# Kernel optimization log

Hardware: AMD Instinct MI355X
Metric: run time of the kernel (lower is better)

The kernel has to match this reference:

```python
import jax, jax.numpy as jnp
import numpy as np

B, T, C, D, P = 8, 512, 32, 128, 1024
EPS = 1e-5

def setup_inputs() -> dict:
    key = jax.random.key(0)
    ks = jax.random.split(key, 11)
    s = 1.0 / np.sqrt(D)
    inp = {
        'x': jax.random.normal(ks[0], (B, T, C, D), jnp.float32),
        'x_mask': jax.random.randint(ks[1], (B, T, C), 0, 2) == 1,
        'p_mask': jax.random.randint(ks[2], (B, T, C), 0, 2) == 1,
        'pos': jax.random.randint(ks[3], (B, T, C), 0, P),
        'pe': jax.random.normal(ks[4], (P, D // 2, 2), jnp.float32),  # complex rpe as [re, im]
        'imp': jax.random.randint(ks[5], (B, T), 0, C),
        'idx_c': jax.random.randint(ks[6], (B, T, C), 0, C),
        'wq_w': jax.random.normal(ks[7], (D, D), jnp.float32) * s,
        'wq_b': jnp.zeros((D,), jnp.float32),
        'wk_w': jax.random.normal(ks[8], (D, D), jnp.float32) * s,
        'wk_b': jnp.zeros((D,), jnp.float32),
        'wv_w': jax.random.normal(ks[9], (D, D), jnp.float32) * s,
        'wv_b': jnp.zeros((D,), jnp.float32),
        'ls_gamma': 1e-5 * jnp.ones((D,), jnp.float32),
        'ln_gamma': jnp.ones((D,), jnp.float32),
        'ln_beta': jnp.zeros((D,), jnp.float32),
    }
    return inp


def _rotate(z, r):
    # z: (b,t,c,d) real; r: (b,t,c,d/2,2) complex multiplier [re,im]
    b, t, c, d = z.shape
    zr = z.reshape(b, t, c, d // 2, 2)
    re = zr[..., 0] * r[..., 0] - zr[..., 1] * r[..., 1]
    im = zr[..., 0] * r[..., 1] + zr[..., 1] * r[..., 0]
    return jnp.stack([re, im], axis=-1).reshape(b, t, c, d)


def reference(x, x_mask, p_mask, pos, pe, imp, idx_c,
              wq_w, wq_b, wk_w, wk_b, wv_w, wv_b,
              ls_gamma, ln_gamma, ln_beta):
    b, t, c, d = x.shape
    # channel selection gather: where x_mask, use per-token important channel
    imp_rep = jnp.broadcast_to(imp[:, :, None], (b, t, c))
    idx = jnp.where(x_mask, imp_rep, idx_c)            # (b,t,c)
    xg = jnp.take_along_axis(x, idx[..., None], axis=2)  # (b,t,c,d)
    # QKV projections (torch Linear: x @ W.T + b)
    q = xg @ wq_w.T + wq_b
    k = xg @ wk_w.T + wk_b
    v = xg @ wv_w.T + wv_b
    # relative PE complex rotation on q,k
    r = pe[pos]                                        # (b,t,c,d/2,2)
    q = _rotate(q, r)
    k = _rotate(k, r)
    # (b,c,t,d) layout; channel acts as head
    qt = q.transpose(0, 2, 1, 3)
    kt = k.transpose(0, 2, 1, 3)
    vt = v.transpose(0, 2, 1, 3)
    scores = jnp.einsum('bcqd,bckd->bcqk', qt, kt) / jnp.sqrt(jnp.float32(d))
    pm = p_mask.transpose(0, 2, 1)                     # (b,c,t)
    mask = pm[:, :, :, None] | pm[:, :, None, :]       # (b,c,t,t)
    attn = jax.nn.softmax(jnp.where(mask, -jnp.inf, scores), axis=-1)
    attn = jnp.nan_to_num(attn)
    xm = x_mask.transpose(0, 2, 1)                     # (b,c,t)
    weight = jnp.where(xm, 1.0 / t, 1.0)
    out = jnp.einsum('bcmn,bcnd->bmcd', attn * weight[:, :, None, :], vt)  # (b,t,c,d)
    # norm_first=False: LN(x + layer_scale(out))
    y = x + ls_gamma * out
    mu = jnp.mean(y, axis=-1, keepdims=True)
    var = jnp.mean(jnp.square(y - mu), axis=-1, keepdims=True)
    return (y - mu) / jnp.sqrt(var + EPS) * ln_gamma + ln_beta
```

## Files before the change

### kernel.cpp

```cpp
#include <hip/hip_runtime.h>
#include <hip/hip_bf16.h>

#define Bb 8
#define Tt 512
#define Cc 32
#define Dd 128
#define SCALE 0.08838834764831845f
#define SROW 520

typedef unsigned int u32;
typedef __hip_bfloat16 bf16;
typedef __attribute__((ext_vector_type(8))) short short8;
typedef __attribute__((ext_vector_type(4))) short short4v;
typedef __attribute__((ext_vector_type(4))) float floatx4;

__device__ __forceinline__ short f2bf(float f) {
    __hip_bfloat16 h = __float2bfloat16(f);
    return *(short*)&h;
}
__device__ __forceinline__ float bf2f(short s) {
    return __uint_as_float(((u32)(unsigned short)s) << 16);
}

__global__ __launch_bounds__(256)
void k_wconv(const float* __restrict__ wq, const float* __restrict__ wk,
             const float* __restrict__ wv, short* __restrict__ Wb)
{
    int g = blockIdx.x * 256 + threadIdx.x;
    int mat = g >> 14, rem = g & 16383;
    const float* src = (mat == 0) ? wq : (mat == 1) ? wk : wv;
    Wb[g] = f2bf(src[rem]);
}

__global__ __launch_bounds__(256)
void k_qkvm(const float* __restrict__ x, const int* __restrict__ xm,
            const int* __restrict__ pos, const float* __restrict__ pe,
            const int* __restrict__ imp, const int* __restrict__ idxc,
            const short* __restrict__ Wb,
            const float* __restrict__ bq, const float* __restrict__ bk,
            const float* __restrict__ bv,
            short* __restrict__ qb, short* __restrict__ kb, short* __restrict__ vb)
{
    const int R0  = blockIdx.x * 64;
    const int b   = R0 >> 14;
    const int t0  = (R0 >> 5) & 511;
    const int tid = threadIdx.x;
    const int w    = tid >> 6;
    const int lane = tid & 63;
    const int quad = lane >> 4;
    const int m    = lane & 15;

    __shared__ short xg[64 * 136];
    __shared__ short ot[64 * 392];

#pragma unroll
    for (int i = 0; i < 8; ++i) {
        int u   = tid + i * 256;
        int row = u >> 5, seg = u & 31;
        int R   = R0 + row;
        int idx = xm[R] ? imp[R >> 5] : idxc[R];
        float4 v = *(const float4*)(x + ((long)(R >> 5) * Cc + idx) * Dd + seg * 4);
        short4v s = {f2bf(v.x), f2bf(v.y), f2bf(v.z), f2bf(v.w)};
        *(short4v*)&xg[row * 136 + seg * 4] = s;
    }

    short8 wf[6][4];
    float  bias_v[6];
#pragma unroll
    for (int mat = 0; mat < 3; ++mat) {
        const float* bp = (mat == 0) ? bq : (mat == 1) ? bk : bv;
#pragma unroll
        for (int h = 0; h < 2; ++h) {
            int sl = mat * 2 + h;
            int ct = h * 4 + w;
            bias_v[sl] = bp[ct * 16 + m];
#pragma unroll
            for (int kk = 0; kk < 4; ++kk)
                wf[sl][kk] = *(const short8*)(Wb + ((long)mat * 128 + ct * 16 + m) * 128
                                              + kk * 32 + quad * 8);
        }
    }
    __syncthreads();

    for (int rt = 0; rt < 4; ++rt) {
        short8 af[4];
#pragma unroll
        for (int kk = 0; kk < 4; ++kk)
            af[kk] = *(const short8*)&xg[(rt * 16 + m) * 136 + kk * 32 + quad * 8];

        floatx4 acc[6];
#pragma unroll
        for (int sl = 0; sl < 6; ++sl) acc[sl] = (floatx4){0.f, 0.f, 0.f, 0.f};
#pragma unroll
        for (int kk = 0; kk < 4; ++kk)
#pragma unroll
            for (int sl = 0; sl < 6; ++sl)
                acc[sl] = __builtin_amdgcn_mfma_f32_16x16x32_bf16(af[kk], wf[sl][kk], acc[sl], 0, 0, 0);

        int po[4];
#pragma unroll
        for (int r = 0; r < 4; ++r) po[r] = pos[R0 + rt * 16 + quad * 4 + r];

#pragma unroll
        for (int sl = 0; sl < 6; ++sl) {
            int mat = sl >> 1;
            int ct  = (sl & 1) * 4 + w;
            int d   = ct * 16 + m;
#pragma unroll
            for (int r = 0; r < 4; ++r) {
                float v = acc[sl][r] + bias_v[sl];
                float p = __shfl_xor(v, 1, 64);
                if (mat < 2) {
                    const float* rp = pe + ((long)po[r] * (Dd / 2) + (d >> 1)) * 2;
                    float r0 = rp[0], r1 = rp[1];
                    v = (d & 1) ? fmaf(p, r1, v * r0) : fmaf(v, r0, -(p * r1));
                    if (mat == 0) v *= SCALE;
                }
                ot[(rt * 16 + quad * 4 + r) * 392 + mat * 128 + d] = f2bf(v);
            }
        }
    }
    __syncthreads();

    short* const mats[3] = {qb, kb, vb};
#pragma unroll
    for (int mat = 0; mat < 3; ++mat) {
        short* dst = mats[mat];
#pragma unroll
        for (int i = 0; i < 4; ++i) {
            int g = tid + i * 256;
            int n = g >> 4, off = (g & 15) * 8;
            int c = n & 31, tl = n >> 5;
            *(short8*)(dst + (((long)(b * Cc + c) * Tt) + t0 + tl) * Dd + off) =
                *(const short8*)&ot[n * 392 + mat * 128 + off];
        }
    }
}

__global__ __launch_bounds__(256)
void k_vt(const short* __restrict__ vb, const int* __restrict__ xm,
          short* __restrict__ vt)
{
    const int head = blockIdx.y;
    const int b    = head >> 5;
    const int c    = head & 31;
    const int t0   = blockIdx.x * 64;
    const int tid  = threadIdx.x;

    __shared__ short tile[64 * 136];
    __shared__ float wks[64];

    if (tid < 64)
        wks[tid] = xm[((long)b * Tt + t0 + tid) * Cc + c] ? (1.0f / Tt) : 1.0f;

    const short* src = vb + ((long)head * Tt + t0) * Dd;
#pragma unroll
    for (int i = 0; i < 4; ++i) {
        int u = tid + i * 256;
        int row = u >> 4, col = (u & 15) * 8;
        *(short8*)&tile[row * 136 + col] = *(const short8*)(src + row * Dd + col);
    }
    __syncthreads();

    short* dst = vt + (long)head * Dd * Tt + t0;
#pragma unroll
    for (int i = 0; i < 4; ++i) {
        int u = tid + i * 256;
        int d = u >> 3, t8 = (u & 7) * 8;
        short8 v;
#pragma unroll
        for (int j = 0; j < 8; ++j)
            v[j] = f2bf(bf2f(tile[(t8 + j) * 136 + d]) * wks[t8 + j]);
        *(short8*)(dst + (long)d * Tt + t8) = v;
    }
}

__global__ __launch_bounds__(512, 4)
void k_attn(const short* __restrict__ qb, const short* __restrict__ kbp,
            const short* __restrict__ vtp, const float* __restrict__ x,
            const int* __restrict__ pm,
            const float* __restrict__ lsg, const float* __restrict__ lng,
            const float* __restrict__ lnb, float* __restrict__ out)
{
    const int l    = blockIdx.y * 256 + blockIdx.x;
    const int xcd  = l & 7;
    const int sws  = l >> 3;
    const int hh   = sws & 7;
    const int tl   = (sws >> 3) & 7;
    const int gg   = sws >> 6;
    const int head = xcd + ((gg * 8 + hh) << 3);
    const int b    = head >> 5;
    const int c    = head & 31;
    const int qt0  = tl * 64;
    const int tid  = threadIdx.x;
    const int w    = tid >> 6;
    const int lane = tid & 63;
    const int quad = lane >> 4;
    const int m    = lane & 15;
    const int d    = w * 16 + m;

    __shared__ short S[64 * SROW];
    __shared__ u32   pkbits[16];
    __shared__ float rlS[64];
    __shared__ float ps1[8][64];
    __shared__ float ps2[8][64];
    __shared__ float mrs[64][2];

    {
        bool v = pm[((long)b * Tt + tid) * Cc + c] != 0;
        unsigned long long bal = __ballot(v);
        if (lane == 0) {
            pkbits[w * 2]     = (u32)bal;
            pkbits[w * 2 + 1] = (u32)(bal >> 32);
        }
    }

    short8 qf[4][4];
#pragma unroll
    for (int qt = 0; qt < 4; ++qt)
#pragma unroll
        for (int kk = 0; kk < 4; ++kk)
            qf[qt][kk] = *(const short8*)(qb + ((long)head * Tt + qt0 + qt * 16 + m) * Dd
                                          + kk * 32 + quad * 8);
    __syncthreads();

    for (int ch = 0; ch < 4; ++ch) {
        int kt = ch * 128 + w * 16 + m;
        const short* kp = kbp + ((long)head * Tt + kt) * Dd + quad * 8;
        floatx4 sc[4];
#pragma unroll
        for (int qt = 0; qt < 4; ++qt) sc[qt] = (floatx4){0.f, 0.f, 0.f, 0.f};
#pragma unroll
        for (int kk = 0; kk < 4; ++kk) {
            short8 bk = *(const short8*)(kp + kk * 32);
            __builtin_amdgcn_s_setprio(1);
#pragma unroll
            for (int qt = 0; qt < 4; ++qt)
                sc[qt] = __builtin_amdgcn_mfma_f32_16x16x32_bf16(qf[qt][kk], bk, sc[qt], 0, 0, 0);
            __builtin_amdgcn_s_setprio(0);
        }
        bool masked = (pkbits[kt >> 5] >> (kt & 31)) & 1;
#pragma unroll
        for (int qt = 0; qt < 4; ++qt)
#pragma unroll
            for (int r = 0; r < 4; ++r)
                S[(qt * 16 + quad * 4 + r) * SROW + kt] = f2bf(masked ? -1e30f : sc[qt][r]);
    }

    const short* vbase = vtp + (long)head * Dd * Tt + ((long)d) * Tt + quad * 8;
    short8 bvbuf[8];
#pragma unroll
    for (int kv = 0; kv < 8; ++kv)
        bvbuf[kv] = *(const short8*)(vbase + kv * 32);

    float xv[4][4];
#pragma unroll
    for (int qt = 0; qt < 4; ++qt)
#pragma unroll
        for (int r = 0; r < 4; ++r) {
            int row = qt * 16 + quad * 4 + r;
            xv[qt][r] = x[(((long)b * Tt + qt0 + row) * Cc + c) * Dd + d];
        }
    __syncthreads();

    {
        int qi = tid >> 3, part = tid & 7;
        short* rowp = &S[qi * SROW + part * 8];
        short8 sv[8];
#pragma unroll
        for (int j = 0; j < 8; ++j) sv[j] = *(short8*)&rowp[j * 64];
        float mx = -1e30f;
#pragma unroll
        for (int j = 0; j < 8; ++j)
#pragma unroll
            for (int e = 0; e < 8; ++e) mx = fmaxf(mx, bf2f(sv[j][e]));
        mx = fmaxf(mx, __shfl_xor(mx, 1, 64));
        mx = fmaxf(mx, __shfl_xor(mx, 2, 64));
        mx = fmaxf(mx, __shfl_xor(mx, 4, 64));
        float lsum = 0.f;
#pragma unroll
        for (int j = 0; j < 8; ++j)
#pragma unroll
            for (int e = 0; e < 8; ++e) {
                float s = bf2f(sv[j][e]);
                float ex = (s <= -1e29f) ? 0.f : __expf(s - mx);
                sv[j][e] = f2bf(ex);
                lsum += ex;
            }
#pragma unroll
        for (int j = 0; j < 8; ++j) *(short8*)&rowp[j * 64] = sv[j];
        lsum += __shfl_xor(lsum, 1, 64);
        lsum += __shfl_xor(lsum, 2, 64);
        lsum += __shfl_xor(lsum, 4, 64);
        if (part == 0) {
            int t = qt0 + qi;
            bool qmask = (pkbits[t >> 5] >> (t & 31)) & 1;
            rlS[qi] = (lsum > 0.f && !qmask) ? 1.0f / lsum : 0.f;
        }
    }
    __syncthreads();

    floatx4 oa[4];
#pragma unroll
    for (int qt = 0; qt < 4; ++qt) oa[qt] = (floatx4){0.f, 0.f, 0.f, 0.f};

#pragma unroll
    for (int kv = 0; kv < 16; ++kv) {
        short8 bv = bvbuf[kv & 7];
        if (kv < 8) bvbuf[kv] = *(const short8*)(vbase + (kv + 8) * 32);
        __builtin_amdgcn_s_setprio(1);
#pragma unroll
        for (int qt = 0; qt < 4; ++qt) {
            short8 ap = *(const short8*)&S[(qt * 16 + m) * SROW + kv * 32 + quad * 8];
            oa[qt] = __builtin_amdgcn_mfma_f32_16x16x32_bf16(ap, bv, oa[qt], 0, 0, 0);
        }
        __builtin_amdgcn_s_setprio(0);
    }

    const float lg = lsg[d];
    float yv[4][4];
#pragma unroll
    for (int qt = 0; qt < 4; ++qt)
#pragma unroll
        for (int r = 0; r < 4; ++r) {
            int row = qt * 16 + quad * 4 + r;
            float val = oa[qt][r] * rlS[row];
            float y = xv[qt][r] + lg * val;
            yv[qt][r] = y;
        }
#pragma unroll
    for (int qt = 0; qt < 4; ++qt)
#pragma unroll
        for (int r = 0; r < 4; ++r) {
            float a = yv[qt][r], bb = yv[qt][r] * yv[qt][r];
            a += __shfl_xor(a, 1, 64); bb += __shfl_xor(bb, 1, 64);
            a += __shfl_xor(a, 2, 64); bb += __shfl_xor(bb, 2, 64);
            a += __shfl_xor(a, 4, 64); bb += __shfl_xor(bb, 4, 64);
            a += __shfl_xor(a, 8, 64); bb += __shfl_xor(bb, 8, 64);
            if (m == 0) {
                ps1[w][qt * 16 + quad * 4 + r] = a;
                ps2[w][qt * 16 + quad * 4 + r] = bb;
            }
        }
    __syncthreads();
    if (tid < 64) {
        float a = 0.f, bb = 0.f;
#pragma unroll
        for (int wv = 0; wv < 8; ++wv) { a += ps1[wv][tid]; bb += ps2[wv][tid]; }
        float mean = a * (1.0f / Dd);
        float var  = bb * (1.0f / Dd) - mean * mean;
        mrs[tid][0] = mean;
        mrs[tid][1] = rsqrtf(var + 1e-5f);
    }
    __syncthreads();

    const float g = lng[d], be = lnb[d];
#pragma unroll
    for (int qt = 0; qt < 4; ++qt)
#pragma unroll
        for (int r = 0; r < 4; ++r) {
            int row = qt * 16 + quad * 4 + r;
            int t = qt0 + row;
            out[(((long)b * Tt + t) * Cc + c) * Dd + d] =
                (yv[qt][r] - mrs[row][0]) * mrs[row][1] * g + be;
        }
}

extern "C" void kernel_launch(void* const* d_in, const int* in_sizes, int n_in,
                              void* d_out, int out_size, void* d_ws, size_t ws_size,
                              hipStream_t stream) {
    const float* x    = (const float*)d_in[0];
    const int* xmask  = (const int*)d_in[1];
    const int* pmask  = (const int*)d_in[2];
    const int* pos    = (const int*)d_in[3];
    const float* pe   = (const float*)d_in[4];
    const int* imp    = (const int*)d_in[5];
    const int* idxc   = (const int*)d_in[6];
    const float* wq_w = (const float*)d_in[7];
    const float* wq_b = (const float*)d_in[8];
    const float* wk_w = (const float*)d_in[9];
    const float* wk_b = (const float*)d_in[10];
    const float* wv_w = (const float*)d_in[11];
    const float* wv_b = (const float*)d_in[12];
    const float* lsg  = (const float*)d_in[13];
    const float* lng  = (const float*)d_in[14];
    const float* lnb  = (const float*)d_in[15];
    float* out = (float*)d_out;

    size_t n = (size_t)Bb * Cc * Tt * Dd;
    short* qb = (short*)d_ws;
    short* kb = qb + n;
    short* vb = kb + n;
    short* vt = vb + n;
    short* Wb = vt + n;

    k_wconv<<<dim3(3 * Dd * Dd / 256), dim3(256), 0, stream>>>(wq_w, wk_w, wv_w, Wb);
    k_qkvm<<<dim3(Bb * Tt * Cc / 64), dim3(256), 0, stream>>>(
        x, xmask, pos, pe, imp, idxc, Wb, wq_b, wk_b, wv_b, qb, kb, vb);
    k_vt<<<dim3(Tt / 64, Bb * Cc), dim3(256), 0, stream>>>(vb, xmask, vt);
    k_attn<<<dim3(256, 8), dim3(512), 0, stream>>>(
        qb, kb, vt, x, pmask, lsg, lng, lnb, out);
}
```

Baseline: 346.7 us.

## Restructure QKV kernel per matrix, swizzle V transpose tile, drop attn prefetch

The QKV projection kernel now processes one matrix at a time with a smaller output staging tile and an occupancy hint. This cuts register and LDS pressure so more blocks can run at once, at the cost of extra barriers and three separate write phases. The V transpose kernel XOR-swizzles its shared tile to avoid LDS bank conflicts on the column reads. The attention kernel drops the V register prefetch, the early x loads and the setprio hints to lower register use, which exposes global-load latency in the PV loop.

```diff
diff --git a/kernel.cpp b/kernel.cpp
--- a/kernel.cpp
+++ b/kernel.cpp
@@ -32,7 +32,7 @@
     Wb[g] = f2bf(src[rem]);
 }
 
-__global__ __launch_bounds__(256)
+__global__ __launch_bounds__(256, 4)
 void k_qkvm(const float* __restrict__ x, const int* __restrict__ xm,
             const int* __restrict__ pos, const float* __restrict__ pe,
             const int* __restrict__ imp, const int* __restrict__ idxc,
@@ -51,7 +51,7 @@
     const int m    = lane & 15;
 
     __shared__ short xg[64 * 136];
-    __shared__ short ot[64 * 392];
+    __shared__ short ot[64 * 136];
 
 #pragma unroll
     for (int i = 0; i < 8; ++i) {
@@ -64,76 +64,77 @@
         *(short4v*)&xg[row * 136 + seg * 4] = s;
     }
 
-    short8 wf[6][4];
-    float  bias_v[6];
+    int po[4][4];
+#pragma unroll
+    for (int rt = 0; rt < 4; ++rt)
+#pragma unroll
+        for (int r = 0; r < 4; ++r)
+            po[rt][r] = pos[R0 + rt * 16 + quad * 4 + r];
+
+    __syncthreads();
+
 #pragma unroll
     for (int mat = 0; mat < 3; ++mat) {
         const float* bp = (mat == 0) ? bq : (mat == 1) ? bk : bv;
+        short*       dst = (mat == 0) ? qb : (mat == 1) ? kb : vb;
+
+        short8 wf[2][4];
+        float  bias_v[2];
 #pragma unroll
         for (int h = 0; h < 2; ++h) {
-            int sl = mat * 2 + h;
             int ct = h * 4 + w;
-            bias_v[sl] = bp[ct * 16 + m];
+            bias_v[h] = bp[ct * 16 + m];
 #pragma unroll
             for (int kk = 0; kk < 4; ++kk)
-                wf[sl][kk] = *(const short8*)(Wb + ((long)mat * 128 + ct * 16 + m) * 128
-                                              + kk * 32 + quad * 8);
-        }
-    }
-    __syncthreads();
-
-    for (int rt = 0; rt < 4; ++rt) {
-        short8 af[4];
-#pragma unroll
-        for (int kk = 0; kk < 4; ++kk)
-            af[kk] = *(const short8*)&xg[(rt * 16 + m) * 136 + kk * 32 + quad * 8];
-
-        floatx4 acc[6];
-#pragma unroll
-        for (int sl = 0; sl < 6; ++sl) acc[sl] = (floatx4){0.f, 0.f, 0.f, 0.f};
-#pragma unroll
-        for (int kk = 0; kk < 4; ++kk)
-#pragma unroll
-            for (int sl = 0; sl < 6; ++sl)
-                acc[sl] = __builtin_amdgcn_mfma_f32_16x16x32_bf16(af[kk], wf[sl][kk], acc[sl], 0, 0, 0);
-
-        int po[4];
-#pragma unroll
-        for (int r = 0; r < 4; ++r) po[r] = pos[R0 + rt * 16 + quad * 4 + r];
-
-#pragma unroll
-        for (int sl = 0; sl < 6; ++sl) {
-            int mat = sl >> 1;
-            int ct  = (sl & 1) * 4 + w;
-            int d   = ct * 16 + m;
-#pragma unroll
-            for (int r = 0; r < 4; ++r) {
-                float v = acc[sl][r] + bias_v[sl];
-                float p = __shfl_xor(v, 1, 64);
-                if (mat < 2) {
-                    const float* rp = pe + ((long)po[r] * (Dd / 2) + (d >> 1)) * 2;
-                    float r0 = rp[0], r1 = rp[1];
-                    v = (d & 1) ? fmaf(p, r1, v * r0) : fmaf(v, r0, -(p * r1));
-                    if (mat == 0) v *= SCALE;
+                wf[h][kk] = *(const short8*)(Wb + ((long)mat * 128 + ct * 16 + m) * 128
+                                             + kk * 32 + quad * 8);
+        }
+
+#pragma unroll
+        for (int rt = 0; rt < 4; ++rt) {
+            short8 af[4];
+#pragma unroll
+            for (int kk = 0; kk < 4; ++kk)
+                af[kk] = *(const short8*)&xg[(rt * 16 + m) * 136 + kk * 32 + quad * 8];
+
+            floatx4 acc[2];
+            acc[0] = (floatx4){0.f, 0.f, 0.f, 0.f};
+            acc[1] = (floatx4){0.f, 0.f, 0.f, 0.f};
+#pragma unroll
+            for (int kk = 0; kk < 4; ++kk)
+#pragma unroll
+                for (int h = 0; h < 2; ++h)
+                    acc[h] = __builtin_amdgcn_mfma_f32_16x16x32_bf16(af[kk], wf[h][kk], acc[h], 0, 0, 0);
+
+#pragma unroll
+            for (int h = 0; h < 2; ++h) {
+                int ct = h * 4 + w;
+                int d  = ct * 16 + m;
+#pragma unroll
+                for (int r = 0; r < 4; ++r) {
+                    float v = acc[h][r] + bias_v[h];
+                    float p = __shfl_xor(v, 1, 64);
+                    if (mat < 2) {
+                        const float* rp = pe + ((long)po[rt][r] * (Dd / 2) + (d >> 1)) * 2;
+                        float r0v = rp[0], r1v = rp[1];
+                        v = (d & 1) ? fmaf(p, r1v, v * r0v) : fmaf(v, r0v, -(p * r1v));
+                        if (mat == 0) v *= SCALE;
+                    }
+                    ot[(rt * 16 + quad * 4 + r) * 136 + d] = f2bf(v);
                 }
-                ot[(rt * 16 + quad * 4 + r) * 392 + mat * 128 + d] = f2bf(v);
             }
         }
-    }
-    __syncthreads();
-
-    short* const mats[3] = {qb, kb, vb};
-#pragma unroll
-    for (int mat = 0; mat < 3; ++mat) {
-        short* dst = mats[mat];
+        __syncthreads();
+
 #pragma unroll
         for (int i = 0; i < 4; ++i) {
             int g = tid + i * 256;
             int n = g >> 4, off = (g & 15) * 8;
             int c = n & 31, tl = n >> 5;
             *(short8*)(dst + (((long)(b * Cc + c) * Tt) + t0 + tl) * Dd + off) =
-                *(const short8*)&ot[n * 392 + mat * 128 + off];
-        }
+                *(const short8*)&ot[n * 136 + off];
+        }
+        __syncthreads();
     }
 }
 
@@ -157,8 +158,9 @@
 #pragma unroll
     for (int i = 0; i < 4; ++i) {
         int u = tid + i * 256;
-        int row = u >> 4, col = (u & 15) * 8;
-        *(short8*)&tile[row * 136 + col] = *(const short8*)(src + row * Dd + col);
+        int row = u >> 4, col8 = u & 15;
+        int c8 = col8 ^ ((row >> 3) & 7);
+        *(short8*)&tile[row * 136 + c8 * 8] = *(const short8*)(src + row * Dd + col8 * 8);
     }
     __syncthreads();
 
@@ -167,10 +169,12 @@
     for (int i = 0; i < 4; ++i) {
         int u = tid + i * 256;
         int d = u >> 3, t8 = (u & 7) * 8;
+        int key = u & 7;
+        int cs = ((d >> 3) ^ key) * 8 + (d & 7);
         short8 v;
 #pragma unroll
         for (int j = 0; j < 8; ++j)
-            v[j] = f2bf(bf2f(tile[(t8 + j) * 136 + d]) * wks[t8 + j]);
+            v[j] = f2bf(bf2f(tile[(t8 + j) * 136 + cs]) * wks[t8 + j]);
         *(short8*)(dst + (long)d * Tt + t8) = v;
     }
 }
@@ -197,7 +201,6 @@
     const int lane = tid & 63;
     const int quad = lane >> 4;
     const int m    = lane & 15;
-    const int d    = w * 16 + m;
 
     __shared__ short S[64 * SROW];
     __shared__ u32   pkbits[16];
@@ -233,11 +236,9 @@
 #pragma unroll
         for (int kk = 0; kk < 4; ++kk) {
             short8 bk = *(const short8*)(kp + kk * 32);
-            __builtin_amdgcn_s_setprio(1);
 #pragma unroll
             for (int qt = 0; qt < 4; ++qt)
                 sc[qt] = __builtin_amdgcn_mfma_f32_16x16x32_bf16(qf[qt][kk], bk, sc[qt], 0, 0, 0);
-            __builtin_amdgcn_s_setprio(0);
         }
         bool masked = (pkbits[kt >> 5] >> (kt & 31)) & 1;
 #pragma unroll
@@ -246,21 +247,6 @@
             for (int r = 0; r < 4; ++r)
                 S[(qt * 16 + quad * 4 + r) * SROW + kt] = f2bf(masked ? -1e30f : sc[qt][r]);
     }
-
-    const short* vbase = vtp + (long)head * Dd * Tt + ((long)d) * Tt + quad * 8;
-    short8 bvbuf[8];
-#pragma unroll
-    for (int kv = 0; kv < 8; ++kv)
-        bvbuf[kv] = *(const short8*)(vbase + kv * 32);
-
-    float xv[4][4];
-#pragma unroll
-    for (int qt = 0; qt < 4; ++qt)
-#pragma unroll
-        for (int r = 0; r < 4; ++r) {
-            int row = qt * 16 + quad * 4 + r;
-            xv[qt][r] = x[(((long)b * Tt + qt0 + row) * Cc + c) * Dd + d];
-        }
     __syncthreads();
 
     {
@@ -304,35 +290,37 @@
 #pragma unroll
     for (int qt = 0; qt < 4; ++qt) oa[qt] = (floatx4){0.f, 0.f, 0.f, 0.f};
 
-#pragma unroll
+    const short* vbase = vtp + (long)head * Dd * Tt + ((long)(w * 16 + m)) * Tt + quad * 8;
     for (int kv = 0; kv < 16; ++kv) {
-        short8 bv = bvbuf[kv & 7];
-        if (kv < 8) bvbuf[kv] = *(const short8*)(vbase + (kv + 8) * 32);
-        __builtin_amdgcn_s_setprio(1);
+        short8 bv = *(const short8*)(vbase + kv * 32);
 #pragma unroll
         for (int qt = 0; qt < 4; ++qt) {
             short8 ap = *(const short8*)&S[(qt * 16 + m) * SROW + kv * 32 + quad * 8];
             oa[qt] = __builtin_amdgcn_mfma_f32_16x16x32_bf16(ap, bv, oa[qt], 0, 0, 0);
         }
-        __builtin_amdgcn_s_setprio(0);
-    }
-
+    }
+
+    const int d = w * 16 + m;
     const float lg = lsg[d];
     float yv[4][4];
+    float s1[4][4], s2[4][4];
 #pragma unroll
     for (int qt = 0; qt < 4; ++qt)
 #pragma unroll
         for (int r = 0; r < 4; ++r) {
             int row = qt * 16 + quad * 4 + r;
+            int t = qt0 + row;
             float val = oa[qt][r] * rlS[row];
-            float y = xv[qt][r] + lg * val;
+            float y = x[(((long)b * Tt + t) * Cc + c) * Dd + d] + lg * val;
             yv[qt][r] = y;
+            s1[qt][r] = y;
+            s2[qt][r] = y * y;
         }
 #pragma unroll
     for (int qt = 0; qt < 4; ++qt)
 #pragma unroll
         for (int r = 0; r < 4; ++r) {
-            float a = yv[qt][r], bb = yv[qt][r] * yv[qt][r];
+            float a = s1[qt][r], bb = s2[qt][r];
             a += __shfl_xor(a, 1, 64); bb += __shfl_xor(bb, 1, 64);
             a += __shfl_xor(a, 2, 64); bb += __shfl_xor(bb, 2, 64);
             a += __shfl_xor(a, 4, 64); bb += __shfl_xor(bb, 4, 64);
```

Result: slower. 366.1 us (+5.6%).
